# Performance work log

Hardware: AMD Instinct MI355X
Metric: run time of the kernel (lower is better)

The kernel has to match this reference:

```python
import jax, jax.numpy as jnp
import numpy as np


def setup_inputs() -> dict:
    key = jax.random.key(0)
    ks = jax.random.split(key, 6)
    B, U, E, D, P = 8, 1024, 1024, 256, 256
    return {
        "u_enc": jax.random.normal(ks[0], (B, U, D), dtype=jnp.float32),
        "e_enc": jax.random.normal(ks[1], (B, E, D), dtype=jnp.float32),
        "pair_enc": jax.random.normal(ks[2], (B, U, E), dtype=jnp.float32),
        "ue_mask": jax.random.uniform(ks[3], (B, U, E), dtype=jnp.float32),
        "w_kernel": jax.random.normal(ks[4], (D, P), dtype=jnp.float32) / np.sqrt(D).astype(np.float32),
        "w_bias": jnp.zeros((P,), dtype=jnp.float32),
        "bpp_w": jnp.ones((), dtype=jnp.float32),
        "bpp_b": jnp.zeros((), dtype=jnp.float32),
    }


def reference(u_enc, e_enc, pair_enc, ue_mask, w_kernel, w_bias, bpp_w, bpp_b):
    # OuterProductUpdate: shared Dense projection of u and e, then outer product.
    u_p = u_enc @ w_kernel + w_bias            # [B,U,P]
    e_p = e_enc @ w_kernel + w_bias            # [B,E,P]
    op = ue_mask * jnp.einsum('bup,bep->bue', u_p, e_p)  # [B,U,E]
    # Sigmoid gate over pair features.
    mask = ue_mask * jax.nn.sigmoid(bpp_w * pair_enc + bpp_b + op)  # [B,U,E]
    # Original: (mask[...,None] * concat(u_rep, e_rep)).sum(axis=(-2,-3)).
    # Algebraically identical without the UxEx2D intermediate:
    #   concat( sum_{u,e} mask * u_enc[u],  sum_{u,e} mask * e_enc[e] )
    u_part = jnp.einsum('bue,bud->bd', mask, u_enc)  # [B,D]
    e_part = jnp.einsum('bue,bed->bd', mask, e_enc)  # [B,D]
    return jnp.concatenate([u_part, e_part], axis=-1)  # [B,2D]
```

## Files before the change

kernel.cpp:

```cpp
#include <hip/hip_runtime.h>

#define BDIM 8
#define UDIM 1024
#define EDIM 1024
#define DDIM 256
#define PDIM 256

typedef __attribute__((ext_vector_type(8))) short bf16x8;
typedef __attribute__((ext_vector_type(4))) float f32x4;
typedef __attribute__((ext_vector_type(4))) ushort u16x4;

__device__ __forceinline__ short f2bf(float x) {
    unsigned u = __float_as_uint(x);
    unsigned r = (u + 0x7FFFu + ((u >> 16) & 1u)) >> 16;
    return (short)r;
}

__device__ __forceinline__ void dma16(const void* g, void* lds) {
    __builtin_amdgcn_global_load_lds(
        (const __attribute__((address_space(1))) unsigned*)g,
        (__attribute__((address_space(3))) unsigned*)lds, 16, 0, 0);
}

#define KEEP(x) asm volatile("" :: "v"(x))

__global__ __launch_bounds__(256) void prep_kernel(
    const float* __restrict__ w, ushort* __restrict__ wT,
    float* __restrict__ out, int out_size)
{
    int k  = threadIdx.x;
    int n0 = blockIdx.x * 4;
    f32x4 wv = *(const f32x4*)(w + (size_t)k * PDIM + n0);
    wT[(size_t)(n0 + 0) * DDIM + k] = (ushort)f2bf(wv[0]);
    wT[(size_t)(n0 + 1) * DDIM + k] = (ushort)f2bf(wv[1]);
    wT[(size_t)(n0 + 2) * DDIM + k] = (ushort)f2bf(wv[2]);
    wT[(size_t)(n0 + 3) * DDIM + k] = (ushort)f2bf(wv[3]);
    int g = blockIdx.x * 256 + k;
    if (g < out_size) out[g] = 0.f;
}

__global__ __launch_bounds__(256) void proj_kernel(
    const float* __restrict__ u_enc, const float* __restrict__ e_enc,
    const ushort* __restrict__ wT, const float* __restrict__ bias,
    ushort* __restrict__ u_p, ushort* __restrict__ e_p)
{
    __shared__ ushort lds_b[64 * 256];

    int bid  = blockIdx.x;
    int lin  = (bid & 7) * 128 + (bid >> 3);
    int row0 = (lin >> 2) * 64;
    int col0 = (lin & 3) * 64;

    const float* A; ushort* C;
    if (row0 < BDIM * UDIM) { A = u_enc; C = u_p; }
    else                    { A = e_enc; C = e_p; row0 -= BDIM * UDIM; }

    int tid  = threadIdx.x;
    int wave = tid >> 6, lane = tid & 63;
    int m = lane & 15, quad = lane >> 4;

    {
        int rl_base = wave * 16;
        int lr = lane >> 5;
        int cb = (lane & 31) * 16;
        #pragma unroll
        for (int j = 0; j < 8; ++j) {
            int rl = rl_base + 2 * j + lr;
            const ushort* src = wT + (size_t)(col0 + rl) * DDIM + ((cb ^ ((rl & 7) << 4)) >> 1);
            dma16(src, &lds_b[(size_t)(rl_base + 2 * j) * DDIM]);
        }
    }

    const float* aptr = A + (size_t)(row0 + wave * 16 + m) * DDIM + quad * 8;
    f32x4 a[16];
    #pragma unroll
    for (int i = 0; i < 8; ++i) {
        a[2 * i]     = *(const f32x4*)(aptr + 32 * i);
        a[2 * i + 1] = *(const f32x4*)(aptr + 32 * i + 4);
    }
    #pragma unroll
    for (int i = 0; i < 16; ++i) KEEP(a[i]);

    asm volatile("s_waitcnt vmcnt(0)" ::: "memory");
    __syncthreads();

    int rowmask = (m & 7) << 4;
    f32x4 acc[4] = {};
    #pragma unroll
    for (int i = 0; i < 8; ++i) {
        bf16x8 af;
        af[0] = f2bf(a[2*i][0]);   af[1] = f2bf(a[2*i][1]);
        af[2] = f2bf(a[2*i][2]);   af[3] = f2bf(a[2*i][3]);
        af[4] = f2bf(a[2*i+1][0]); af[5] = f2bf(a[2*i+1][1]);
        af[6] = f2bf(a[2*i+1][2]); af[7] = f2bf(a[2*i+1][3]);
        #pragma unroll
        for (int nt = 0; nt < 4; ++nt) {
            int elem = (nt * 16 + m) * DDIM + (((quad * 16 + 64 * i) ^ rowmask) >> 1);
            bf16x8 bfr = *(const bf16x8*)(lds_b + elem);
            acc[nt] = __builtin_amdgcn_mfma_f32_16x16x32_bf16(af, bfr, acc[nt], 0, 0, 0);
        }
    }

    #pragma unroll
    for (int r = 0; r < 4; ++r) {
        int row = row0 + wave * 16 + quad * 4 + r;
        u16x4 pk;
        #pragma unroll
        for (int nt = 0; nt < 4; ++nt)
            pk[nt] = (ushort)f2bf(acc[nt][r] + bias[col0 + nt * 16 + m]);
        *(u16x4*)(C + (size_t)row * PDIM + col0 + 4 * m) = pk;
    }
}

__global__ __launch_bounds__(256) void fused_kernel(
    const ushort* __restrict__ u_p, const ushort* __restrict__ e_p,
    const float* __restrict__ pair_enc, const float* __restrict__ ue_mask,
    const float* __restrict__ bpp_w_p, const float* __restrict__ bpp_b_p,
    float* __restrict__ row_part ,
    float* __restrict__ col_part )
{
    __shared__ ushort lds_e[64 * 256];
    __shared__ float lds_pair[64][64];
    __shared__ float lds_mask[64][64];
    __shared__ float colred[4][64];

    int bid  = blockIdx.x;
    int b    = bid & 7;
    int tile = bid >> 3;
    int iu = tile >> 4, ie = tile & 15;
    int u0 = iu * 64, e0 = ie * 64;

    int tid  = threadIdx.x;
    int wave = tid >> 6, lane = tid & 63;
    int m = lane & 15, quad = lane >> 4;

    const float* pm = pair_enc + (size_t)b * UDIM * EDIM;
    const float* mm = ue_mask  + (size_t)b * UDIM * EDIM;
    const ushort* eb = e_p + (size_t)b * EDIM * PDIM;

    {
        int rl_base = wave * 16;
        int lr = lane >> 5;
        int cb = (lane & 31) * 16;
        #pragma unroll
        for (int j = 0; j < 8; ++j) {
            int rl = rl_base + 2 * j + lr;
            const ushort* src = eb + (size_t)(e0 + rl) * PDIM + ((cb ^ ((rl & 7) << 4)) >> 1);
            dma16(src, &lds_e[(size_t)(rl_base + 2 * j) * PDIM]);
        }
    }

    {
        int lr = lane >> 4;
        int lc = (lane & 15) * 4;
        #pragma unroll
        for (int j = 0; j < 4; ++j) {
            int r0 = wave * 16 + j * 4;
            size_t goff = (size_t)(u0 + r0 + lr) * EDIM + e0 + lc;
            dma16(pm + goff, &lds_pair[r0][0]);
            dma16(mm + goff, &lds_mask[r0][0]);
        }
    }

    const ushort* Au = u_p + (size_t)b * UDIM * PDIM + (size_t)(u0 + wave * 16 + m) * PDIM + quad * 8;
    bf16x8 af[8];
    #pragma unroll
    for (int i = 0; i < 8; ++i) af[i] = *(const bf16x8*)(Au + 32 * i);
    #pragma unroll
    for (int i = 0; i < 8; ++i) KEEP(af[i]);

    float bw = bpp_w_p[0], bb = bpp_b_p[0];

    asm volatile("s_waitcnt vmcnt(0)" ::: "memory");
    __syncthreads();

    int rowmask = (m & 7) << 4;
    f32x4 acc[4] = {};
    #pragma unroll
    for (int i = 0; i < 8; ++i) {
        #pragma unroll
        for (int nt = 0; nt < 4; ++nt) {
            int elem = (nt * 16 + m) * PDIM + (((quad * 16 + 64 * i) ^ rowmask) >> 1);
            bf16x8 bfr = *(const bf16x8*)(lds_e + elem);
            acc[nt] = __builtin_amdgcn_mfma_f32_16x16x32_bf16(af[i], bfr, acc[nt], 0, 0, 0);
        }
    }

    float rsum[4] = {0.f, 0.f, 0.f, 0.f};
    float csum[4] = {0.f, 0.f, 0.f, 0.f};
    #pragma unroll
    for (int r = 0; r < 4; ++r) {
        int row = wave * 16 + quad * 4 + r;
        #pragma unroll
        for (int nt = 0; nt < 4; ++nt) {
            int col = nt * 16 + m;
            float mv = lds_mask[row][col];
            float pv = lds_pair[row][col];
            float arg = bw * pv + bb + mv * acc[nt][r];
            float s = mv / (1.f + __expf(-arg));
            rsum[r]  += s;
            csum[nt] += s;
        }
    }

    #pragma unroll
    for (int r = 0; r < 4; ++r) {
        float v = rsum[r];
        v += __shfl_xor(v, 1); v += __shfl_xor(v, 2);
        v += __shfl_xor(v, 4); v += __shfl_xor(v, 8);
        if (m == 0)
            row_part[((size_t)b * 16 + ie) * UDIM + u0 + wave * 16 + quad * 4 + r] = v;
    }

    #pragma unroll
    for (int nt = 0; nt < 4; ++nt) {
        float v = csum[nt];
        v += __shfl_xor(v, 16); v += __shfl_xor(v, 32);
        if (quad == 0) colred[wave][nt * 16 + m] = v;
    }
    __syncthreads();

    if (tid < 64) {
        float v = colred[0][tid] + colred[1][tid] + colred[2][tid] + colred[3][tid];
        col_part[((size_t)b * 16 + iu) * EDIM + e0 + tid] = v;
    }
}

__global__ __launch_bounds__(256) void finish_kernel(
    const float* __restrict__ u_enc, const float* __restrict__ e_enc,
    const float* __restrict__ row_part, const float* __restrict__ col_part,
    float* __restrict__ out)
{
    __shared__ float s_lds[32];

    int b = blockIdx.x;
    int half = blockIdx.y;
    int chunk = blockIdx.z;
    int d = threadIdx.x;

    const float* enc  = half ? e_enc   : u_enc;
    const float* part = half ? col_part : row_part;

    int base = chunk * 32;
    if (d < 32) {
        float s = 0.f;
        #pragma unroll
        for (int p = 0; p < 16; ++p)
            s += part[((size_t)b * 16 + p) * UDIM + base + d];
        s_lds[d] = s;
    }

    float ev[32];
    #pragma unroll
    for (int j = 0; j < 32; ++j)
        ev[j] = enc[(size_t)(b * UDIM + base + j) * DDIM + d];
    #pragma unroll
    for (int j = 0; j < 32; ++j) KEEP(ev[j]);

    __syncthreads();

    float acc = 0.f;
    #pragma unroll
    for (int j = 0; j < 32; ++j)
        acc += s_lds[j] * ev[j];

    atomicAdd(&out[(size_t)b * 2 * DDIM + half * DDIM + d], acc);
}

extern "C" void kernel_launch(void* const* d_in, const int* in_sizes, int n_in,
                              void* d_out, int out_size, void* d_ws, size_t ws_size,
                              hipStream_t stream)
{
    const float* u_enc    = (const float*)d_in[0];
    const float* e_enc    = (const float*)d_in[1];
    const float* pair_enc = (const float*)d_in[2];
    const float* ue_mask  = (const float*)d_in[3];
    const float* w_kernel = (const float*)d_in[4];
    const float* w_bias   = (const float*)d_in[5];
    const float* bpp_w    = (const float*)d_in[6];
    const float* bpp_b    = (const float*)d_in[7];
    float* out = (float*)d_out;

    ushort* u_p = (ushort*)d_ws;
    ushort* e_p = u_p + (size_t)BDIM * UDIM * PDIM;
    ushort* wT  = e_p + (size_t)BDIM * EDIM * PDIM;
    float* row_part = (float*)(wT + (size_t)DDIM * PDIM);
    float* col_part = row_part + (size_t)BDIM * 16 * UDIM;

    prep_kernel<<<dim3(64), 256, 0, stream>>>(w_kernel, wT, out, out_size);

    proj_kernel<<<dim3(1024), 256, 0, stream>>>(u_enc, e_enc, wT, w_bias, u_p, e_p);

    fused_kernel<<<dim3(2048), 256, 0, stream>>>(u_p, e_p, pair_enc, ue_mask,
                                                 bpp_w, bpp_b, row_part, col_part);

    finish_kernel<<<dim3(BDIM, 2, 32), 256, 0, stream>>>(u_enc, e_enc, row_part, col_part, out);
}
```

Measured before the change: 148.6 us.

## Load pair/mask tiles directly into registers via permuted e-row layout

Drops the LDS staging of the pair_enc and ue_mask tiles. Instead, the rows of e_p loaded into LDS are permuted so that each lane's MFMA output columns match a contiguous 4-float chunk, and each lane loads its pair and mask values as 16-byte vector loads straight from global memory into registers. The column-reduction index is remapped to match. This saves 32KB of LDS per block, which may raise occupancy, and removes an LDS round trip, at the cost of more registers and a less regular global access pattern.

```diff
diff --git a/kernel.cpp b/kernel.cpp
--- a/kernel.cpp
+++ b/kernel.cpp
@@ -120,8 +120,6 @@
     float* __restrict__ col_part )
 {
     __shared__ ushort lds_e[64 * 256];
-    __shared__ float lds_pair[64][64];
-    __shared__ float lds_mask[64][64];
     __shared__ float colred[4][64];
 
     int bid  = blockIdx.x;
@@ -139,26 +137,14 @@
     const ushort* eb = e_p + (size_t)b * EDIM * PDIM;
 
     {
-        int rl_base = wave * 16;
         int lr = lane >> 5;
         int cb = (lane & 31) * 16;
         #pragma unroll
         for (int j = 0; j < 8; ++j) {
-            int rl = rl_base + 2 * j + lr;
-            const ushort* src = eb + (size_t)(e0 + rl) * PDIM + ((cb ^ ((rl & 7) << 4)) >> 1);
-            dma16(src, &lds_e[(size_t)(rl_base + 2 * j) * PDIM]);
-        }
-    }
-
-    {
-        int lr = lane >> 4;
-        int lc = (lane & 15) * 4;
-        #pragma unroll
-        for (int j = 0; j < 4; ++j) {
-            int r0 = wave * 16 + j * 4;
-            size_t goff = (size_t)(u0 + r0 + lr) * EDIM + e0 + lc;
-            dma16(pm + goff, &lds_pair[r0][0]);
-            dma16(mm + goff, &lds_mask[r0][0]);
+            int rl = wave * 16 + 2 * j + lr;
+            int esrc = e0 + ((rl & 15) << 2) + (rl >> 4);
+            const ushort* src = eb + (size_t)esrc * PDIM + ((cb ^ ((rl & 7) << 4)) >> 1);
+            dma16(src, &lds_e[(size_t)(wave * 16 + 2 * j) * PDIM]);
         }
     }
 
@@ -168,6 +154,19 @@
     for (int i = 0; i < 8; ++i) af[i] = *(const bf16x8*)(Au + 32 * i);
     #pragma unroll
     for (int i = 0; i < 8; ++i) KEEP(af[i]);
+
+    {
+    }
+    const float* pmRow = pm + (size_t)(u0 + wave * 16 + quad * 4) * EDIM + e0 + 4 * m;
+    const float* mmRow = mm + (size_t)(u0 + wave * 16 + quad * 4) * EDIM + e0 + 4 * m;
+    f32x4 pv4[4], mv4[4];
+    #pragma unroll
+    for (int r = 0; r < 4; ++r) {
+        pv4[r] = *(const f32x4*)(pmRow + (size_t)r * EDIM);
+        mv4[r] = *(const f32x4*)(mmRow + (size_t)r * EDIM);
+    }
+    #pragma unroll
+    for (int r = 0; r < 4; ++r) { KEEP(pv4[r]); KEEP(mv4[r]); }
 
     float bw = bpp_w_p[0], bb = bpp_b_p[0];
 
@@ -190,13 +189,11 @@
     float csum[4] = {0.f, 0.f, 0.f, 0.f};
     #pragma unroll
     for (int r = 0; r < 4; ++r) {
-        int row = wave * 16 + quad * 4 + r;
         #pragma unroll
         for (int nt = 0; nt < 4; ++nt) {
-            int col = nt * 16 + m;
-            float mv = lds_mask[row][col];
-            float pv = lds_pair[row][col];
-            float arg = bw * pv + bb + mv * acc[nt][r];
+            float mv = mv4[r][nt];
+            float pvv = pv4[r][nt];
+            float arg = bw * pvv + bb + mv * acc[nt][r];
             float s = mv / (1.f + __expf(-arg));
             rsum[r]  += s;
             csum[nt] += s;
@@ -216,7 +213,7 @@
     for (int nt = 0; nt < 4; ++nt) {
         float v = csum[nt];
         v += __shfl_xor(v, 16); v += __shfl_xor(v, 32);
-        if (quad == 0) colred[wave][nt * 16 + m] = v;
+        if (quad == 0) colred[wave][4 * m + nt] = v;
     }
     __syncthreads();
 
```

New measurement: 148.8 us. Within noise of the previous version (+0.1%).
